# Performance work log

Measured on AMD Instinct MI355X. Metric: run time of the kernel, lower is better.

Reference implementation:

```python
import jax, jax.numpy as jnp
import numpy as np

NEIGHBOR_NUM = 4


def reference(vertices, feature_map, sample_idx):
    # vertices: (bs, n, 3), feature_map: (bs, n, c), sample_idx: (pool_num,)
    # pairwise squared distances: ||a||^2 + ||b||^2 - 2 a.b
    inner = jnp.einsum('bnd,bmd->bnm', vertices, vertices)  # (bs, n, n)
    quad = jnp.sum(vertices * vertices, axis=2)             # (bs, n)
    distance = -2.0 * inner + quad[:, None, :] + quad[:, :, None]
    # k+1 smallest distances (self is nearest); lax.top_k finds largest, so negate
    _, neighbor_index = jax.lax.top_k(-distance, NEIGHBOR_NUM + 1)
    neighbor_index = neighbor_index[:, :, 1:]               # drop self -> (bs, n, k)
    # gather neighbor features per batch: (bs, n, k, c)
    neighbor_feature = jax.vmap(lambda f, idx: f[idx])(feature_map, neighbor_index)
    pooled_feature = jnp.max(neighbor_feature, axis=2)      # (bs, n, c)
    vertices_pool = vertices[:, sample_idx, :]              # (bs, pool_num, 3)
    feature_map_pool = pooled_feature[:, sample_idx, :]     # (bs, pool_num, c)
    return vertices_pool, feature_map_pool


def setup_inputs() -> dict:
    key = jax.random.key(0)
    k1, k2 = jax.random.split(key)
    bs, n, c = 8, 4096, 256
    pool_num = n // 4
    vertices = jax.random.normal(k1, (bs, n, 3), dtype=jnp.float32)
    feature_map = jax.random.normal(k2, (bs, n, c), dtype=jnp.float32)
    sample_idx = jnp.arange(pool_num, dtype=jnp.int32)
    return {"vertices": vertices, "feature_map": feature_map, "sample_idx": sample_idx}
```

## Files before the change

kernel.cpp:

```cpp
#include <hip/hip_runtime.h>
#include <stdint.h>

#define BATCH 8
#define NPTS  4096
#define CH    256
#define QN    1024
#define WAVES_PER_BLOCK 16
#define BLOCK (WAVES_PER_BLOCK * 64)
#define BLOCKS_PER_BATCH (QN / WAVES_PER_BLOCK)

__device__ __forceinline__ float fmul(float a, float b) { return __fmul_rn(a, b); }
__device__ __forceinline__ float fadd(float a, float b) { return __fadd_rn(a, b); }

__device__ __forceinline__ void cswap(uint64_t& lo, uint64_t& hi) {
  uint64_t mn = hi < lo ? hi : lo;
  uint64_t mx = hi < lo ? lo : hi;
  lo = mn; hi = mx;
}

__device__ __forceinline__ float cdist(const float4 vq, const float4 v) {
  float dot = fadd(fadd(fmul(vq.x, v.x), fmul(vq.y, v.y)), fmul(vq.z, v.z));
  return fadd(fadd(fmul(-2.0f, dot), v.w), vq.w);
}

__device__ __forceinline__ uint64_t mkkey(float d, int c) {
  uint32_t bb = __float_as_uint(d);
  bb ^= (uint32_t)((int32_t)bb >> 31) | 0x80000000u;
  return ((uint64_t)bb << 32) | (uint32_t)c;
}

__global__ __launch_bounds__(BLOCK, 8) void knn_pool_kernel(
    const float* __restrict__ verts,
    const float* __restrict__ feat,
    const int*   __restrict__ sidx,
    float* __restrict__ outV,
    float* __restrict__ outF)
{
  extern __shared__ float4 sv[];

  const int batch = blockIdx.x / BLOCKS_PER_BATCH;
  const int qblk  = blockIdx.x % BLOCKS_PER_BATCH;
  const float* vb = verts + (size_t)batch * (NPTS * 3);

  for (int c = threadIdx.x; c < NPTS; c += BLOCK) {
    float x = vb[c * 3 + 0];
    float y = vb[c * 3 + 1];
    float z = vb[c * 3 + 2];
    float q = fadd(fadd(fmul(x, x), fmul(y, y)), fmul(z, z));
    sv[c] = make_float4(x, y, z, q);
  }
  __syncthreads();

  const int wave = threadIdx.x >> 6;
  const int lane = threadIdx.x & 63;
  const int i = qblk * WAVES_PER_BLOCK + wave;
  const int n = sidx[i];
  const float4 vq = sv[n];
  const float4* svp = sv + lane;

  uint64_t a0 = ~0ull, a1 = ~0ull;
#pragma unroll 8
  for (int t = 0; t < NPTS / 64; ++t) {
    float4 v = svp[t * 64];
    uint64_t key = mkkey(cdist(vq, v), lane + t * 64);
    a1 = key < a1 ? key : a1;
    cswap(a0, a1);
  }

  uint64_t prev = 0;
  uint64_t nb1 = 0, nb2 = 0, nb3 = 0, nb4 = 0;
#pragma unroll
  for (int r = 0; r < 5; ++r) {
    uint64_t cand = a0 > prev ? a0 : (a1 > prev ? a1 : ~0ull);
#pragma unroll
    for (int s = 32; s >= 1; s >>= 1) {
      uint64_t o = (uint64_t)__shfl_xor((long long)cand, s, 64);
      if (o < cand) cand = o;
    }
    if (r == 1) nb1 = cand;
    if (r == 2) nb2 = cand;
    if (r == 3) nb3 = cand;
    if (r == 4) nb4 = cand;
    prev = cand;
  }

  bool bad = (a1 < nb4);
  if (__any(bad)) {
    uint64_t b0 = ~0ull, b1 = ~0ull, b2 = ~0ull, b3 = ~0ull, b4 = ~0ull;
    for (int t = 0; t < NPTS / 64; ++t) {
      float4 v = svp[t * 64];
      uint64_t key = mkkey(cdist(vq, v), lane + t * 64);
      b4 = key < b4 ? key : b4;
      cswap(b3, b4);
      cswap(b2, b3);
      cswap(b1, b2);
      cswap(b0, b1);
    }
    prev = 0;
#pragma unroll
    for (int r = 0; r < 5; ++r) {
      uint64_t cand = b0 > prev ? b0
                    : b1 > prev ? b1
                    : b2 > prev ? b2
                    : b3 > prev ? b3
                    : b4 > prev ? b4 : ~0ull;
#pragma unroll
      for (int s = 32; s >= 1; s >>= 1) {
        uint64_t o = (uint64_t)__shfl_xor((long long)cand, s, 64);
        if (o < cand) cand = o;
      }
      if (r == 1) nb1 = cand;
      if (r == 2) nb2 = cand;
      if (r == 3) nb3 = cand;
      if (r == 4) nb4 = cand;
      prev = cand;
    }
  }

  const int n1 = (int)(uint32_t)nb1;
  const int n2 = (int)(uint32_t)nb2;
  const int n3 = (int)(uint32_t)nb3;
  const int n4 = (int)(uint32_t)nb4;

  const float* fb = feat + (size_t)batch * NPTS * CH;
  const int col = lane * 4;
  float4 f1 = *(const float4*)(fb + (size_t)n1 * CH + col);
  float4 f2 = *(const float4*)(fb + (size_t)n2 * CH + col);
  float4 f3 = *(const float4*)(fb + (size_t)n3 * CH + col);
  float4 f4 = *(const float4*)(fb + (size_t)n4 * CH + col);
  float4 r;
  r.x = fmaxf(fmaxf(f1.x, f2.x), fmaxf(f3.x, f4.x));
  r.y = fmaxf(fmaxf(f1.y, f2.y), fmaxf(f3.y, f4.y));
  r.z = fmaxf(fmaxf(f1.z, f2.z), fmaxf(f3.z, f4.z));
  r.w = fmaxf(fmaxf(f1.w, f2.w), fmaxf(f3.w, f4.w));
  *(float4*)(outF + ((size_t)batch * QN + i) * CH + col) = r;

  if (lane < 3) {
    outV[((size_t)batch * QN + i) * 3 + lane] = vb[(size_t)n * 3 + lane];
  }
}

extern "C" void kernel_launch(void* const* d_in, const int* in_sizes, int n_in,
                              void* d_out, int out_size, void* d_ws, size_t ws_size,
                              hipStream_t stream) {
  const float* verts = (const float*)d_in[0];
  const float* feat  = (const float*)d_in[1];
  const int*   sidx  = (const int*)d_in[2];
  float* outV = (float*)d_out;
  float* outF = (float*)d_out + (size_t)BATCH * QN * 3;

  dim3 grid(BATCH * BLOCKS_PER_BATCH);
  dim3 block(BLOCK);
  size_t lds_bytes = (size_t)NPTS * sizeof(float4);
  knn_pool_kernel<<<grid, block, lds_bytes, stream>>>(verts, feat, sidx, outV, outF);
}
```

Baseline: 44.19 us.

## Process four queries per wave to reuse each LDS vertex load

Each wave now handles four query points at once, so every float4 read from shared memory feeds four distance computations and top-2 updates. This cuts LDS read traffic per query by four. Blocks shrink from 16 waves to 4 while covering the same 16 queries, and the LDS array becomes static. The cost is more registers per thread from the per-query arrays, lower occupancy, and fallback rescans that now run serially per query inside a wave.

```diff
diff --git a/kernel.cpp b/kernel.cpp
--- a/kernel.cpp
+++ b/kernel.cpp
@@ -5,9 +5,11 @@
 #define NPTS  4096
 #define CH    256
 #define QN    1024
-#define WAVES_PER_BLOCK 16
+#define QPW   4
+#define WAVES_PER_BLOCK 4
 #define BLOCK (WAVES_PER_BLOCK * 64)
-#define BLOCKS_PER_BATCH (QN / WAVES_PER_BLOCK)
+#define QPB   (WAVES_PER_BLOCK * QPW)
+#define BLOCKS_PER_BATCH (QN / QPB)
 
 __device__ __forceinline__ float fmul(float a, float b) { return __fmul_rn(a, b); }
 __device__ __forceinline__ float fadd(float a, float b) { return __fadd_rn(a, b); }
@@ -29,15 +31,24 @@
   return ((uint64_t)bb << 32) | (uint32_t)c;
 }
 
-__global__ __launch_bounds__(BLOCK, 8) void knn_pool_kernel(
+__device__ __forceinline__ uint64_t wave_min(uint64_t cand) {
+#pragma unroll
+  for (int s = 32; s >= 1; s >>= 1) {
+    uint64_t o = (uint64_t)__shfl_xor((long long)cand, s, 64);
+    if (o < cand) cand = o;
+  }
+  return cand;
+}
+
+__shared__ float4 sv[NPTS];
+
+__global__ __launch_bounds__(BLOCK) void knn_pool_kernel(
     const float* __restrict__ verts,
     const float* __restrict__ feat,
     const int*   __restrict__ sidx,
     float* __restrict__ outV,
     float* __restrict__ outF)
 {
-  extern __shared__ float4 sv[];
-
   const int batch = blockIdx.x / BLOCKS_PER_BATCH;
   const int qblk  = blockIdx.x % BLOCKS_PER_BATCH;
   const float* vb = verts + (size_t)batch * (NPTS * 3);
@@ -53,90 +64,99 @@
 
   const int wave = threadIdx.x >> 6;
   const int lane = threadIdx.x & 63;
-  const int i = qblk * WAVES_PER_BLOCK + wave;
-  const int n = sidx[i];
-  const float4 vq = sv[n];
+  const int qbase = qblk * QPB + wave * QPW;
   const float4* svp = sv + lane;
 
-  uint64_t a0 = ~0ull, a1 = ~0ull;
-#pragma unroll 8
+  int   nq[QPW];
+  float4 vq[QPW];
+#pragma unroll
+  for (int q = 0; q < QPW; ++q) {
+    nq[q] = sidx[qbase + q];
+    vq[q] = sv[nq[q]];
+  }
+
+  uint64_t a0[QPW], a1[QPW];
+#pragma unroll
+  for (int q = 0; q < QPW; ++q) { a0[q] = ~0ull; a1[q] = ~0ull; }
+
+#pragma unroll 4
   for (int t = 0; t < NPTS / 64; ++t) {
     float4 v = svp[t * 64];
-    uint64_t key = mkkey(cdist(vq, v), lane + t * 64);
-    a1 = key < a1 ? key : a1;
-    cswap(a0, a1);
+    const int c = lane + t * 64;
+#pragma unroll
+    for (int q = 0; q < QPW; ++q) {
+      uint64_t key = mkkey(cdist(vq[q], v), c);
+      a1[q] = key < a1[q] ? key : a1[q];
+      cswap(a0[q], a1[q]);
+    }
   }
 
-  uint64_t prev = 0;
-  uint64_t nb1 = 0, nb2 = 0, nb3 = 0, nb4 = 0;
+  int n1[QPW], n2[QPW], n3[QPW], n4[QPW];
 #pragma unroll
-  for (int r = 0; r < 5; ++r) {
-    uint64_t cand = a0 > prev ? a0 : (a1 > prev ? a1 : ~0ull);
-#pragma unroll
-    for (int s = 32; s >= 1; s >>= 1) {
-      uint64_t o = (uint64_t)__shfl_xor((long long)cand, s, 64);
-      if (o < cand) cand = o;
-    }
-    if (r == 1) nb1 = cand;
-    if (r == 2) nb2 = cand;
-    if (r == 3) nb3 = cand;
-    if (r == 4) nb4 = cand;
-    prev = cand;
-  }
-
-  bool bad = (a1 < nb4);
-  if (__any(bad)) {
-    uint64_t b0 = ~0ull, b1 = ~0ull, b2 = ~0ull, b3 = ~0ull, b4 = ~0ull;
-    for (int t = 0; t < NPTS / 64; ++t) {
-      float4 v = svp[t * 64];
-      uint64_t key = mkkey(cdist(vq, v), lane + t * 64);
-      b4 = key < b4 ? key : b4;
-      cswap(b3, b4);
-      cswap(b2, b3);
-      cswap(b1, b2);
-      cswap(b0, b1);
-    }
-    prev = 0;
+  for (int q = 0; q < QPW; ++q) {
+    uint64_t prev = 0, nb1 = 0, nb2 = 0, nb3 = 0, nb4 = 0;
 #pragma unroll
     for (int r = 0; r < 5; ++r) {
-      uint64_t cand = b0 > prev ? b0
-                    : b1 > prev ? b1
-                    : b2 > prev ? b2
-                    : b3 > prev ? b3
-                    : b4 > prev ? b4 : ~0ull;
-#pragma unroll
-      for (int s = 32; s >= 1; s >>= 1) {
-        uint64_t o = (uint64_t)__shfl_xor((long long)cand, s, 64);
-        if (o < cand) cand = o;
-      }
+      uint64_t cand = a0[q] > prev ? a0[q] : (a1[q] > prev ? a1[q] : ~0ull);
+      cand = wave_min(cand);
       if (r == 1) nb1 = cand;
       if (r == 2) nb2 = cand;
       if (r == 3) nb3 = cand;
       if (r == 4) nb4 = cand;
       prev = cand;
     }
+    if (__any(a1[q] < nb4)) {
+      uint64_t b0 = ~0ull, b1 = ~0ull, b2 = ~0ull, b3 = ~0ull, b4 = ~0ull;
+      for (int t = 0; t < NPTS / 64; ++t) {
+        float4 v = svp[t * 64];
+        uint64_t key = mkkey(cdist(vq[q], v), lane + t * 64);
+        b4 = key < b4 ? key : b4;
+        cswap(b3, b4); cswap(b2, b3); cswap(b1, b2); cswap(b0, b1);
+      }
+      prev = 0;
+#pragma unroll
+      for (int r = 0; r < 5; ++r) {
+        uint64_t cand = b0 > prev ? b0
+                      : b1 > prev ? b1
+                      : b2 > prev ? b2
+                      : b3 > prev ? b3
+                      : b4 > prev ? b4 : ~0ull;
+        cand = wave_min(cand);
+        if (r == 1) nb1 = cand;
+        if (r == 2) nb2 = cand;
+        if (r == 3) nb3 = cand;
+        if (r == 4) nb4 = cand;
+        prev = cand;
+      }
+    }
+    n1[q] = (int)(uint32_t)nb1;
+    n2[q] = (int)(uint32_t)nb2;
+    n3[q] = (int)(uint32_t)nb3;
+    n4[q] = (int)(uint32_t)nb4;
   }
-
-  const int n1 = (int)(uint32_t)nb1;
-  const int n2 = (int)(uint32_t)nb2;
-  const int n3 = (int)(uint32_t)nb3;
-  const int n4 = (int)(uint32_t)nb4;
 
   const float* fb = feat + (size_t)batch * NPTS * CH;
   const int col = lane * 4;
-  float4 f1 = *(const float4*)(fb + (size_t)n1 * CH + col);
-  float4 f2 = *(const float4*)(fb + (size_t)n2 * CH + col);
-  float4 f3 = *(const float4*)(fb + (size_t)n3 * CH + col);
-  float4 f4 = *(const float4*)(fb + (size_t)n4 * CH + col);
-  float4 r;
-  r.x = fmaxf(fmaxf(f1.x, f2.x), fmaxf(f3.x, f4.x));
-  r.y = fmaxf(fmaxf(f1.y, f2.y), fmaxf(f3.y, f4.y));
-  r.z = fmaxf(fmaxf(f1.z, f2.z), fmaxf(f3.z, f4.z));
-  r.w = fmaxf(fmaxf(f1.w, f2.w), fmaxf(f3.w, f4.w));
-  *(float4*)(outF + ((size_t)batch * QN + i) * CH + col) = r;
+#pragma unroll
+  for (int q = 0; q < QPW; ++q) {
+    float4 f1 = *(const float4*)(fb + (size_t)n1[q] * CH + col);
+    float4 f2 = *(const float4*)(fb + (size_t)n2[q] * CH + col);
+    float4 f3 = *(const float4*)(fb + (size_t)n3[q] * CH + col);
+    float4 f4 = *(const float4*)(fb + (size_t)n4[q] * CH + col);
+    float4 r;
+    r.x = fmaxf(fmaxf(f1.x, f2.x), fmaxf(f3.x, f4.x));
+    r.y = fmaxf(fmaxf(f1.y, f2.y), fmaxf(f3.y, f4.y));
+    r.z = fmaxf(fmaxf(f1.z, f2.z), fmaxf(f3.z, f4.z));
+    r.w = fmaxf(fmaxf(f1.w, f2.w), fmaxf(f3.w, f4.w));
+    *(float4*)(outF + ((size_t)batch * QN + qbase + q) * CH + col) = r;
+  }
 
-  if (lane < 3) {
-    outV[((size_t)batch * QN + i) * 3 + lane] = vb[(size_t)n * 3 + lane];
+#pragma unroll
+  for (int q = 0; q < QPW; ++q) {
+    if (lane < 3) {
+      float val = lane == 0 ? vq[q].x : (lane == 1 ? vq[q].y : vq[q].z);
+      outV[((size_t)batch * QN + qbase + q) * 3 + lane] = val;
+    }
   }
 }
 
@@ -151,6 +171,5 @@
 
   dim3 grid(BATCH * BLOCKS_PER_BATCH);
   dim3 block(BLOCK);
-  size_t lds_bytes = (size_t)NPTS * sizeof(float4);
-  knn_pool_kernel<<<grid, block, lds_bytes, stream>>>(verts, feat, sidx, outV, outF);
+  knn_pool_kernel<<<grid, block, 0, stream>>>(verts, feat, sidx, outV, outF);
 }
```

After: 54.47 us. +23.3%, slower.
